# Optimization experiments

Hardware: AMD Instinct MI355X
Metric: run time of the kernel (lower is better)

Reference implementation:

```python
import jax, jax.numpy as jnp
import numpy as np

N, C, E = 2048, 512, 8192
EPS = 1e-5
MASK_FILL = -10000.0


def layer_norm(h, g, b):
    m = jnp.mean(h, axis=-1, keepdims=True)
    v = jnp.mean(jnp.square(h - m), axis=-1, keepdims=True)
    return (h - m) * jax.lax.rsqrt(v + EPS) * g + b


def setup_inputs() -> dict:
    key = jax.random.key(0)
    ks = jax.random.split(key, 20)
    s = 1.0 / np.sqrt(C)
    inp = {
        "x": jax.random.normal(ks[0], (N, C), jnp.float32),
        "edge_index": jax.random.randint(ks[1], (2, E), 0, N, jnp.int64),
        "edge_attr": jax.random.normal(ks[2], (E, C), jnp.float32),
        "edge_masks": jax.random.randint(ks[3], (E, E), 0, 2, jnp.int32).astype(bool),
        # GraphConv.nn: Linear(C, C)
        "W_nn": jax.random.normal(ks[4], (C, C), jnp.float32) * s,
        "b_nn": jax.random.normal(ks[5], (C,), jnp.float32) * s,
        # att_nn: Linear(3C, C) -> Tanh -> Linear(C, 1, bias=False) -> LeakyReLU(0.2)
        "W_att1": jax.random.normal(ks[6], (C, 3 * C), jnp.float32) * (1.0 / np.sqrt(3 * C)),
        "b_att1": jax.random.normal(ks[7], (C,), jnp.float32) * s,
        "w_att2": jax.random.normal(ks[8], (C,), jnp.float32) * s,
        # root weight [C, C] and bias [C]
        "root": jax.random.normal(ks[9], (C, C), jnp.float32) * s,
        "bias": jax.random.normal(ks[10], (C,), jnp.float32) * s,
        # graph_block: LayerNorms + Linear(C, C)
        "gamma1": jnp.ones((C,), jnp.float32),
        "beta1": jnp.zeros((C,), jnp.float32),
        "gamma2": jnp.ones((C,), jnp.float32),
        "beta2": jnp.zeros((C,), jnp.float32),
        "W_lin": jax.random.normal(ks[11], (C, C), jnp.float32) * s,
        "b_lin": jax.random.normal(ks[12], (C,), jnp.float32) * s,
    }
    return inp


def reference(x, edge_index, edge_attr, edge_masks, W_nn, b_nn, W_att1, b_att1,
              w_att2, root, bias, gamma1, beta1, gamma2, beta2, W_lin, b_lin):
    src = edge_index[0]  # x_j (source)
    dst = edge_index[1]  # x_i (target), also aggregation index

    # shared linear on gathered endpoints and edge attrs  [E, C]
    h_i = x[dst] @ W_nn.T + b_nn
    h_j = x[src] @ W_nn.T + b_nn
    h_e = edge_attr @ W_nn.T + b_nn

    # attention MLP (dropout in eval mode = identity)
    cat = jnp.concatenate([h_i, h_j, h_e], axis=1)          # [E, 3C]
    hid = jnp.tanh(cat @ W_att1.T + b_att1)                  # [E, C]
    s = hid @ w_att2                                         # [E]
    s = jax.nn.leaky_relu(s, 0.2)

    # row-wise masked softmax of the broadcast score vector; keep only diagonal
    logits = jnp.where(edge_masks, s[None, :], MASK_FILL)    # [E, E]
    lse = jax.scipy.special.logsumexp(logits, axis=1)        # [E]
    diag_logit = jnp.where(jnp.diagonal(edge_masks), s, MASK_FILL)
    att_diag = jnp.exp(diag_logit - lse)                     # [E]

    msg = h_j * att_diag[:, None]                            # [E, C]
    aggr = jax.ops.segment_sum(msg, dst, num_segments=N)     # [N, C]

    out = aggr + x @ root + bias                             # update()

    # graph_block wrapper
    x1 = layer_norm(out, gamma1, beta1)
    x2 = layer_norm(x1 + (x1 @ W_lin.T + b_lin), gamma2, beta2)
    return x2
```

## Files before the change

### kernel.cpp

```cpp
#include <hip/hip_runtime.h>
#include <stdint.h>
#include <stddef.h>

#define NN 2048
#define CD 512
#define EE 8192

typedef unsigned short u16;
typedef __attribute__((ext_vector_type(8))) short short8;
typedef __attribute__((ext_vector_type(4))) float floatx4;

__device__ inline u16 f2bf(float f) {
    uint32_t u = __float_as_uint(f);
    u += 0x7FFFu + ((u >> 16) & 1u);
    return (u16)(u >> 16);
}
__device__ inline float bf2f(u16 h) { return __uint_as_float(((uint32_t)h) << 16); }

__global__ __launch_bounds__(256) void prep_kernel(
    const float* __restrict__ x, const float* __restrict__ ea,
    const float* __restrict__ Wnn, const float* __restrict__ Wlin,
    const float* __restrict__ root, const float* __restrict__ Watt1,
    u16* __restrict__ xb, u16* __restrict__ eb, u16* __restrict__ Bcat,
    u16* __restrict__ WnnTb, u16* __restrict__ Wlinb, u16* __restrict__ Wpackb)
{
    size_t i4 = ((size_t)blockIdx.x * 256 + threadIdx.x) * 4;
    auto cvt4 = [](const float* src, u16* dst, size_t idx) {
        float4 v = *(const float4*)(src + idx);
        ushort4 o; o.x = f2bf(v.x); o.y = f2bf(v.y); o.z = f2bf(v.z); o.w = f2bf(v.w);
        *(ushort4*)(dst + idx) = o;
    };
    if (i4 < 1048576) { cvt4(x, xb, i4); return; }
    i4 -= 1048576;
    if (i4 < 4194304) { cvt4(ea, eb, i4); return; }
    i4 -= 4194304;
    if (i4 < 262144) { cvt4(Wnn, Bcat, i4); return; }
    i4 -= 262144;
    if (i4 < 262144) {
        int c = (int)(i4 >> 9), k = (int)(i4 & 511);
        ushort4 o;
        o.x = f2bf(root[(size_t)(k + 0) * 512 + c]);
        o.y = f2bf(root[(size_t)(k + 1) * 512 + c]);
        o.z = f2bf(root[(size_t)(k + 2) * 512 + c]);
        o.w = f2bf(root[(size_t)(k + 3) * 512 + c]);
        *(ushort4*)(Bcat + 262144 + i4) = o; return;
    }
    i4 -= 262144;
    if (i4 < 262144) {
        int k = (int)(i4 >> 9), t = (int)(i4 & 511);
        ushort4 o;
        o.x = f2bf(Wnn[(size_t)(t + 0) * 512 + k]);
        o.y = f2bf(Wnn[(size_t)(t + 1) * 512 + k]);
        o.z = f2bf(Wnn[(size_t)(t + 2) * 512 + k]);
        o.w = f2bf(Wnn[(size_t)(t + 3) * 512 + k]);
        *(ushort4*)(WnnTb + i4) = o; return;
    }
    i4 -= 262144;
    if (i4 < 262144) { cvt4(Wlin, Wlinb, i4); return; }
    i4 -= 262144;
    {
        int cp = (int)(i4 >> 9), t = (int)(i4 & 511);
        const float* sp = Watt1 + (size_t)(cp & 511) * 1536 + (cp >> 9) * 512 + t;
        float4 v = *(const float4*)sp;
        ushort4 o; o.x = f2bf(v.x); o.y = f2bf(v.y); o.z = f2bf(v.z); o.w = f2bf(v.w);
        *(ushort4*)(Wpackb + i4) = o;
    }
}

__global__ __launch_bounds__(256) void bbvec_kernel(
    const float* __restrict__ Watt1, const float* __restrict__ bnn,
    const float* __restrict__ batt1, float* __restrict__ bb)
{
    const int c = blockIdx.x, tid = threadIdx.x;
    const float* row = Watt1 + (size_t)c * 1536;
    float partial = 0.0f;
#pragma unroll
    for (int t = tid; t < 1536; t += 256) partial += row[t] * bnn[t & 511];
    for (int o = 32; o; o >>= 1) partial += __shfl_down(partial, o);
    __shared__ float red[4];
    if ((tid & 63) == 0) red[tid >> 6] = partial;
    __syncthreads();
    if (tid == 0) bb[c] = batt1[c] + red[0] + red[1] + red[2] + red[3];
}

template<int BM, int BN>
__device__ inline void gemm_core(const u16* __restrict__ A, const u16* __restrict__ B,
                                 int bm, int bn, int tid, u16* As, u16* Bs,
                                 floatx4 (&acc)[BM / 32][BN / 32])
{
    constexpr int K = 512, BK = 32, WM = BM / 2, WN = BN / 2, FM = WM / 16, FN = WN / 16;
    const int wave = tid >> 6, lane = tid & 63;
    const int wm = wave >> 1, wn = wave & 1;
    const int lrow = lane & 15, lk = lane >> 4;
    constexpr int ALOADS = (BM * BK) / (256 * 8);
    constexpr int BLOADS = (BN * BK) / (256 * 8);
    for (int k0 = 0; k0 < K; k0 += BK) {
        __syncthreads();
#pragma unroll
        for (int c = 0; c < ALOADS; ++c) {
            int e = c * 2048 + tid * 8;
            int row = e >> 5, col = e & 31;
            __builtin_amdgcn_global_load_lds(
                (const __attribute__((address_space(1))) void*)(A + (size_t)(bm * BM + row) * K + k0 + col),
                (__attribute__((address_space(3))) void*)(&As[e]), 16, 0, 0);
        }
#pragma unroll
        for (int c = 0; c < BLOADS; ++c) {
            int e = c * 2048 + tid * 8;
            int row = e >> 5, col = e & 31;
            __builtin_amdgcn_global_load_lds(
                (const __attribute__((address_space(1))) void*)(B + (size_t)(bn * BN + row) * K + k0 + col),
                (__attribute__((address_space(3))) void*)(&Bs[e]), 16, 0, 0);
        }
        __syncthreads();
        short8 af[FM], bfr[FN];
#pragma unroll
        for (int i = 0; i < FM; ++i)
            af[i] = *(const short8*)(&As[(wm * WM + i * 16 + lrow) * BK + lk * 8]);
#pragma unroll
        for (int j = 0; j < FN; ++j)
            bfr[j] = *(const short8*)(&Bs[(wn * WN + j * 16 + lrow) * BK + lk * 8]);
#pragma unroll
        for (int i = 0; i < FM; ++i)
#pragma unroll
            for (int j = 0; j < FN; ++j)
                acc[i][j] = __builtin_amdgcn_mfma_f32_16x16x32_bf16(af[i], bfr[j], acc[i][j], 0, 0, 0);
    }
}

template<int BM, int BN, bool OUT_BF16, bool BIAS>
__global__ __launch_bounds__(256) void gemm_bt(
    const u16* __restrict__ A, const u16* __restrict__ B,
    void* __restrict__ Cout, const float* __restrict__ bias, int Nc)
{
    __shared__ __align__(16) u16 As[BM * 32];
    __shared__ __align__(16) u16 Bs[BN * 32];
    constexpr int WM = BM / 2, WN = BN / 2, FM = WM / 16, FN = WN / 16;
    floatx4 acc[FM][FN] = {};
    const int tid = threadIdx.x, bm = blockIdx.x, bn = blockIdx.y;
    gemm_core<BM, BN>(A, B, bm, bn, tid, As, Bs, acc);
    const int wave = tid >> 6, lane = tid & 63, wm = wave >> 1, wn = wave & 1;
    const int lrow = lane & 15, lk = lane >> 4;
#pragma unroll
    for (int i = 0; i < FM; ++i)
#pragma unroll
        for (int j = 0; j < FN; ++j) {
            const int col = bn * BN + wn * WN + j * 16 + lrow;
            const float bv = BIAS ? bias[col] : 0.0f;
#pragma unroll
            for (int r = 0; r < 4; ++r) {
                const int row = bm * BM + wm * WM + i * 16 + lk * 4 + r;
                const float v = acc[i][j][r] + bv;
                if (OUT_BF16) ((u16*)Cout)[(size_t)row * Nc + col] = f2bf(v);
                else          ((float*)Cout)[(size_t)row * Nc + col] = v;
            }
        }
}

__global__ __launch_bounds__(256) void node_gemm(
    const u16* __restrict__ A, const u16* __restrict__ B,
    const float* __restrict__ bnn, const float* __restrict__ bias,
    u16* __restrict__ Hb, float* __restrict__ OUT1, float* __restrict__ G12)
{
    __shared__ __align__(16) u16 As[128 * 32];
    __shared__ __align__(16) u16 Bs[128 * 32];
    floatx4 acc[4][4] = {};
    const int tid = threadIdx.x, bm = blockIdx.x, bn = blockIdx.y;
    gemm_core<128, 128>(A, B, bm, bn, tid, As, Bs, acc);
    const int wave = tid >> 6, lane = tid & 63, wm = wave >> 1, wn = wave & 1;
    const int lrow = lane & 15, lk = lane >> 4;
#pragma unroll
    for (int i = 0; i < 4; ++i)
#pragma unroll
        for (int j = 0; j < 4; ++j) {
            const int colg = bn * 128 + wn * 64 + j * 16 + lrow;
#pragma unroll
            for (int r = 0; r < 4; ++r) {
                const int row = bm * 128 + wm * 64 + i * 16 + lk * 4 + r;
                const float v = acc[i][j][r];
                if (bn < 4) {
                    Hb[(size_t)row * 512 + colg] = f2bf(v + bnn[colg]);
                } else if (bn < 8) {
                    const int c = colg - 512;
                    OUT1[(size_t)row * 512 + c] = v + bias[c];
                } else {
                    G12[(size_t)row * 1024 + (colg - 1024)] = v;
                }
            }
        }
}

__global__ __launch_bounds__(256) void edge_gemm_score(
    const u16* __restrict__ A, const u16* __restrict__ B,
    const float* __restrict__ G12, const int* __restrict__ ei,
    const float* __restrict__ bb, const float* __restrict__ w2,
    float* __restrict__ sraw)
{
    __shared__ __align__(16) u16 As[128 * 32];
    __shared__ __align__(16) u16 Bs[128 * 32];
    floatx4 acc[4][4] = {};
    const int tid = threadIdx.x, bm = blockIdx.x, bn = blockIdx.y;
    gemm_core<128, 128>(A, B, bm, bn, tid, As, Bs, acc);
    const int wave = tid >> 6, lane = tid & 63, wm = wave >> 1, wn = wave & 1;
    const int lrow = lane & 15, lk = lane >> 4;
#pragma unroll
    for (int i = 0; i < 4; ++i) {
#pragma unroll
        for (int r = 0; r < 4; ++r) {
            const int e = bm * 128 + wm * 64 + i * 16 + lk * 4 + r;
            const int sn = ei[e], dn = ei[EE + e];
            float sp = 0.0f;
#pragma unroll
            for (int j = 0; j < 4; ++j) {
                const int col = bn * 128 + wn * 64 + j * 16 + lrow;
                const float v = acc[i][j][r]
                              + G12[(size_t)dn * 1024 + col]
                              + G12[(size_t)sn * 1024 + 512 + col]
                              + bb[col];
                sp += tanhf(v) * w2[col];
            }
#pragma unroll
            for (int m = 1; m < 16; m <<= 1) sp += __shfl_xor(sp, m);
            if (lrow == 0) atomicAdd(sraw + e, sp);
        }
    }
}

__global__ __launch_bounds__(1024) void softmax_prep(
    const float* __restrict__ sraw, float* __restrict__ p)
{
    const int tid = threadIdx.x;
    float sv[8];
    float m = -3.0e38f;
#pragma unroll
    for (int k = 0; k < 8; ++k) {
        float v = sraw[k * 1024 + tid];
        v = (v >= 0.0f) ? v : 0.2f * v;
        sv[k] = v; m = fmaxf(m, v);
    }
    for (int o = 32; o; o >>= 1) m = fmaxf(m, __shfl_down(m, o));
    __shared__ float red[16];
    if ((tid & 63) == 0) red[tid >> 6] = m;
    __syncthreads();
    float M = red[0];
#pragma unroll
    for (int k = 1; k < 16; ++k) M = fmaxf(M, red[k]);
#pragma unroll
    for (int k = 0; k < 8; ++k) p[k * 1024 + tid] = __expf(sv[k] - M);
}

__global__ __launch_bounds__(256) void lse_att(
    const unsigned char* __restrict__ mask, const float* __restrict__ p,
    float* __restrict__ att)
{
    const int i0 = blockIdx.x * 4, tid = threadIdx.x;
    float sums[4] = {0.0f, 0.0f, 0.0f, 0.0f};
#pragma unroll
    for (int c = 0; c < 2; ++c) {
        const int base = c * 4096 + tid * 16;
        float pv[16];
#pragma unroll
        for (int q = 0; q < 4; ++q)
            *(float4*)(pv + q * 4) = *(const float4*)(p + base + q * 4);
#pragma unroll
        for (int rr = 0; rr < 4; ++rr) {
            uint4 mw = *(const uint4*)(mask + (size_t)(i0 + rr) * EE + base);
            uint32_t w[4] = { mw.x, mw.y, mw.z, mw.w };
            float s = 0.0f;
#pragma unroll
            for (int q = 0; q < 4; ++q) {
                s += pv[q * 4 + 0] * (float)((w[q]      ) & 1u);
                s += pv[q * 4 + 1] * (float)((w[q] >>  8) & 1u);
                s += pv[q * 4 + 2] * (float)((w[q] >> 16) & 1u);
                s += pv[q * 4 + 3] * (float)((w[q] >> 24) & 1u);
            }
            sums[rr] += s;
        }
    }
#pragma unroll
    for (int rr = 0; rr < 4; ++rr)
        for (int o = 32; o; o >>= 1) sums[rr] += __shfl_down(sums[rr], o);
    __shared__ float red[4][4];
    if ((tid & 63) == 0) {
#pragma unroll
        for (int rr = 0; rr < 4; ++rr) red[rr][tid >> 6] = sums[rr];
    }
    __syncthreads();
    if (tid < 4) {
        const int i = i0 + tid;
        const float total = red[tid][0] + red[tid][1] + red[tid][2] + red[tid][3];
        const unsigned char diag = mask[(size_t)i * EE + i];
        float a;
        if (total > 0.0f) a = diag ? (p[i] / total) : 0.0f;
        else              a = 1.0f / (float)EE;
        att[i] = a;
    }
}

__global__ __launch_bounds__(256) void aggr_kernel(
    const u16* __restrict__ Hb, const int* __restrict__ ei,
    const float* __restrict__ att, float* __restrict__ OUT1)
{
    const int e = blockIdx.x;
    const float a = att[e];
    if (a == 0.0f) return;
    const int sn = ei[e], dn = ei[EE + e];
    const u16* h = Hb + (size_t)sn * 512;
    float* o = OUT1 + (size_t)dn * 512;
    const int c = threadIdx.x * 2;
    const uint32_t hv = *(const uint32_t*)(h + c);
    atomicAdd(o + c,     a * bf2f((u16)(hv & 0xffffu)));
    atomicAdd(o + c + 1, a * bf2f((u16)(hv >> 16)));
}

template<bool RESID, bool WRITE_BF16>
__global__ __launch_bounds__(256) void ln_kernel(
    const float* __restrict__ in, const float* __restrict__ resid,
    const float* __restrict__ gamma, const float* __restrict__ beta,
    float* __restrict__ outF, u16* __restrict__ outB)
{
    const int n = blockIdx.x, tid = threadIdx.x;
    const size_t rowoff = (size_t)n * 512;
    float2 v = *(const float2*)(in + rowoff + tid * 2);
    float a0 = v.x, a1 = v.y;
    if (RESID) {
        float2 r = *(const float2*)(resid + rowoff + tid * 2);
        a0 += r.x; a1 += r.y;
    }
    float sum = a0 + a1, sq = a0 * a0 + a1 * a1;
    for (int o = 32; o; o >>= 1) { sum += __shfl_down(sum, o); sq += __shfl_down(sq, o); }
    __shared__ float rs_[4], rq_[4];
    if ((tid & 63) == 0) { rs_[tid >> 6] = sum; rq_[tid >> 6] = sq; }
    __syncthreads();
    sum = rs_[0] + rs_[1] + rs_[2] + rs_[3];
    sq  = rq_[0] + rq_[1] + rq_[2] + rq_[3];
    const float mean = sum * (1.0f / 512.0f);
    const float var  = sq * (1.0f / 512.0f) - mean * mean;
    const float rstd = rsqrtf(var + 1e-5f);
    const int c0 = tid * 2;
    const float y0 = (a0 - mean) * rstd * gamma[c0]     + beta[c0];
    const float y1 = (a1 - mean) * rstd * gamma[c0 + 1] + beta[c0 + 1];
    *(float2*)(outF + rowoff + c0) = make_float2(y0, y1);
    if (WRITE_BF16) { outB[rowoff + c0] = f2bf(y0); outB[rowoff + c0 + 1] = f2bf(y1); }
}

extern "C" void kernel_launch(void* const* d_in, const int* in_sizes, int n_in,
                              void* d_out, int out_size, void* d_ws, size_t ws_size,
                              hipStream_t stream)
{
    const float* x     = (const float*)d_in[0];
    const int*   ei    = (const int*)d_in[1];
    const float* ea    = (const float*)d_in[2];
    const unsigned char* mask = (const unsigned char*)d_in[3];
    const float* Wnn   = (const float*)d_in[4];
    const float* bnn   = (const float*)d_in[5];
    const float* Watt1 = (const float*)d_in[6];
    const float* batt1 = (const float*)d_in[7];
    const float* watt2 = (const float*)d_in[8];
    const float* root  = (const float*)d_in[9];
    const float* bias  = (const float*)d_in[10];
    const float* gam1  = (const float*)d_in[11];
    const float* bet1  = (const float*)d_in[12];
    const float* gam2  = (const float*)d_in[13];
    const float* bet2  = (const float*)d_in[14];
    const float* Wlin  = (const float*)d_in[15];
    const float* blin  = (const float*)d_in[16];
    float* out = (float*)d_out;

    char* w = (char*)d_ws;
    auto take = [&](size_t bytes) -> char* {
        char* pp = w; w += (bytes + 255) & ~(size_t)255; return pp;
    };
    u16*   xb     = (u16*)take((size_t)NN * CD * 2);
    u16*   eb     = (u16*)take((size_t)EE * CD * 2);
    u16*   Wpackb = (u16*)take((size_t)1536 * CD * 2);
    u16*   WnnTb  = (u16*)take((size_t)CD * CD * 2);
    u16*   Wlinb  = (u16*)take((size_t)CD * CD * 2);
    u16*   Bcat   = (u16*)take((size_t)2560 * CD * 2);
    u16*   Hb     = (u16*)take((size_t)NN * CD * 2);
    float* G12    = (float*)take((size_t)NN * 1024 * 4);
    float* OUT1   = (float*)take((size_t)NN * CD * 4);
    float* sraw   = (float*)take((size_t)EE * 4);
    float* pbuf   = (float*)take((size_t)EE * 4);
    float* attb   = (float*)take((size_t)EE * 4);
    float* bb     = (float*)take((size_t)CD * 4);
    float* x1     = (float*)take((size_t)NN * CD * 4);
    u16*   x1b    = (u16*)take((size_t)NN * CD * 2);
    float* Tbuf   = (float*)take((size_t)NN * CD * 4);

    hipMemsetAsync(sraw, 0, (size_t)EE * 4, stream);
    prep_kernel<<<6912, 256, 0, stream>>>(x, ea, Wnn, Wlin, root, Watt1,
                                          xb, eb, Bcat, WnnTb, Wlinb, Wpackb);
    bbvec_kernel<<<512, 256, 0, stream>>>(Watt1, bnn, batt1, bb);
    gemm_bt<64, 128, true, false><<<dim3(24, 4), 256, 0, stream>>>(
        Wpackb, WnnTb, Bcat + (size_t)1024 * 512, nullptr, 512);
    node_gemm<<<dim3(16, 16), 256, 0, stream>>>(xb, Bcat, bnn, bias, Hb, OUT1, G12);
    edge_gemm_score<<<dim3(64, 4), 256, 0, stream>>>(
        eb, Bcat + (size_t)2048 * 512, G12, ei, bb, watt2, sraw);
    softmax_prep<<<1, 1024, 0, stream>>>(sraw, pbuf);
    lse_att<<<2048, 256, 0, stream>>>(mask, pbuf, attb);
    aggr_kernel<<<EE, 256, 0, stream>>>(Hb, ei, attb, OUT1);
    ln_kernel<false, true><<<NN, 256, 0, stream>>>(OUT1, nullptr, gam1, bet1, x1, x1b);
    gemm_bt<64, 128, false, true><<<dim3(32, 4), 256, 0, stream>>>(x1b, Wlinb, Tbuf, blin, 512);
    ln_kernel<true, false><<<NN, 256, 0, stream>>>(Tbuf, x1, gam2, bet2, out, nullptr);
}
```

Before: 457.9 us.

## Fuse softmax, attention and aggregation; full-width edge GEMM; fuse linear with LN2

Folds the bias-vector kernel into the prep kernel and restructures the edge GEMM so each block computes all 512 output columns for 32 edges. That removes the atomic score accumulation and the memset. The separate softmax-max pass is dropped: exp is applied directly to the scores inside a combined LSE/attention/aggregation kernel, which then scatters the messages. The final linear layer is fused with the residual add and the second LayerNorm in one kernel. The aim is fewer launches and fewer intermediate buffers. The cost is lower block counts for the wide-tile GEMMs and no max subtraction, which could overflow exp for large scores.

```diff
diff --git a/kernel.cpp b/kernel.cpp
--- a/kernel.cpp
+++ b/kernel.cpp
@@ -21,9 +21,24 @@
     const float* __restrict__ x, const float* __restrict__ ea,
     const float* __restrict__ Wnn, const float* __restrict__ Wlin,
     const float* __restrict__ root, const float* __restrict__ Watt1,
+    const float* __restrict__ bnn, const float* __restrict__ batt1,
     u16* __restrict__ xb, u16* __restrict__ eb, u16* __restrict__ Bcat,
-    u16* __restrict__ WnnTb, u16* __restrict__ Wlinb, u16* __restrict__ Wpackb)
-{
+    u16* __restrict__ WnnTb, u16* __restrict__ Wlinb, u16* __restrict__ Wpackb,
+    float* __restrict__ bb)
+{
+    if (blockIdx.x >= 6912) {
+        const int c = blockIdx.x - 6912, tid = threadIdx.x;
+        const float* row = Watt1 + (size_t)c * 1536;
+        float partial = 0.0f;
+#pragma unroll
+        for (int t = tid; t < 1536; t += 256) partial += row[t] * bnn[t & 511];
+        for (int o = 32; o; o >>= 1) partial += __shfl_down(partial, o);
+        __shared__ float red[4];
+        if ((tid & 63) == 0) red[tid >> 6] = partial;
+        __syncthreads();
+        if (tid == 0) bb[c] = batt1[c] + red[0] + red[1] + red[2] + red[3];
+        return;
+    }
     size_t i4 = ((size_t)blockIdx.x * 256 + threadIdx.x) * 4;
     auto cvt4 = [](const float* src, u16* dst, size_t idx) {
         float4 v = *(const float4*)(src + idx);
@@ -67,50 +82,56 @@
     }
 }
 
-__global__ __launch_bounds__(256) void bbvec_kernel(
-    const float* __restrict__ Watt1, const float* __restrict__ bnn,
-    const float* __restrict__ batt1, float* __restrict__ bb)
-{
-    const int c = blockIdx.x, tid = threadIdx.x;
-    const float* row = Watt1 + (size_t)c * 1536;
-    float partial = 0.0f;
-#pragma unroll
-    for (int t = tid; t < 1536; t += 256) partial += row[t] * bnn[t & 511];
-    for (int o = 32; o; o >>= 1) partial += __shfl_down(partial, o);
-    __shared__ float red[4];
-    if ((tid & 63) == 0) red[tid >> 6] = partial;
-    __syncthreads();
-    if (tid == 0) bb[c] = batt1[c] + red[0] + red[1] + red[2] + red[3];
-}
-
-template<int BM, int BN>
+template<int BM, int BN, int WR, int WC>
 __device__ inline void gemm_core(const u16* __restrict__ A, const u16* __restrict__ B,
                                  int bm, int bn, int tid, u16* As, u16* Bs,
-                                 floatx4 (&acc)[BM / 32][BN / 32])
-{
-    constexpr int K = 512, BK = 32, WM = BM / 2, WN = BN / 2, FM = WM / 16, FN = WN / 16;
+                                 floatx4 (&acc)[(BM / WR) / 16][(BN / WC) / 16])
+{
+    constexpr int K = 512, BK = 32;
+    constexpr int WM = BM / WR, WN = BN / WC;
+    constexpr int FM = WM / 16, FN = WN / 16;
+    constexpr int ATH = BM * BK / 8;
+    constexpr int BTH = BN * BK / 8;
     const int wave = tid >> 6, lane = tid & 63;
-    const int wm = wave >> 1, wn = wave & 1;
+    const int wm = wave / WC, wn = wave % WC;
     const int lrow = lane & 15, lk = lane >> 4;
-    constexpr int ALOADS = (BM * BK) / (256 * 8);
-    constexpr int BLOADS = (BN * BK) / (256 * 8);
     for (int k0 = 0; k0 < K; k0 += BK) {
         __syncthreads();
-#pragma unroll
-        for (int c = 0; c < ALOADS; ++c) {
-            int e = c * 2048 + tid * 8;
-            int row = e >> 5, col = e & 31;
-            __builtin_amdgcn_global_load_lds(
-                (const __attribute__((address_space(1))) void*)(A + (size_t)(bm * BM + row) * K + k0 + col),
-                (__attribute__((address_space(3))) void*)(&As[e]), 16, 0, 0);
-        }
-#pragma unroll
-        for (int c = 0; c < BLOADS; ++c) {
-            int e = c * 2048 + tid * 8;
-            int row = e >> 5, col = e & 31;
-            __builtin_amdgcn_global_load_lds(
-                (const __attribute__((address_space(1))) void*)(B + (size_t)(bn * BN + row) * K + k0 + col),
-                (__attribute__((address_space(3))) void*)(&Bs[e]), 16, 0, 0);
+        if constexpr (ATH >= 256) {
+#pragma unroll
+            for (int c = 0; c < ATH / 256; ++c) {
+                int e = c * 2048 + tid * 8;
+                int row = e >> 5, col = e & 31;
+                __builtin_amdgcn_global_load_lds(
+                    (const __attribute__((address_space(1))) void*)(A + (size_t)(bm * BM + row) * K + k0 + col),
+                    (__attribute__((address_space(3))) void*)(&As[e]), 16, 0, 0);
+            }
+        } else {
+            if (tid < ATH) {
+                int e = tid * 8;
+                int row = e >> 5, col = e & 31;
+                __builtin_amdgcn_global_load_lds(
+                    (const __attribute__((address_space(1))) void*)(A + (size_t)(bm * BM + row) * K + k0 + col),
+                    (__attribute__((address_space(3))) void*)(&As[e]), 16, 0, 0);
+            }
+        }
+        if constexpr (BTH >= 256) {
+#pragma unroll
+            for (int c = 0; c < BTH / 256; ++c) {
+                int e = c * 2048 + tid * 8;
+                int row = e >> 5, col = e & 31;
+                __builtin_amdgcn_global_load_lds(
+                    (const __attribute__((address_space(1))) void*)(B + (size_t)(bn * BN + row) * K + k0 + col),
+                    (__attribute__((address_space(3))) void*)(&Bs[e]), 16, 0, 0);
+            }
+        } else {
+            if (tid < BTH) {
+                int e = tid * 8;
+                int row = e >> 5, col = e & 31;
+                __builtin_amdgcn_global_load_lds(
+                    (const __attribute__((address_space(1))) void*)(B + (size_t)(bn * BN + row) * K + k0 + col),
+                    (__attribute__((address_space(3))) void*)(&Bs[e]), 16, 0, 0);
+            }
         }
         __syncthreads();
         short8 af[FM], bfr[FN];
@@ -135,21 +156,21 @@
 {
     __shared__ __align__(16) u16 As[BM * 32];
     __shared__ __align__(16) u16 Bs[BN * 32];
-    constexpr int WM = BM / 2, WN = BN / 2, FM = WM / 16, FN = WN / 16;
+    constexpr int FM = (BM / 2) / 16, FN = (BN / 2) / 16;
     floatx4 acc[FM][FN] = {};
     const int tid = threadIdx.x, bm = blockIdx.x, bn = blockIdx.y;
-    gemm_core<BM, BN>(A, B, bm, bn, tid, As, Bs, acc);
+    gemm_core<BM, BN, 2, 2>(A, B, bm, bn, tid, As, Bs, acc);
     const int wave = tid >> 6, lane = tid & 63, wm = wave >> 1, wn = wave & 1;
     const int lrow = lane & 15, lk = lane >> 4;
 #pragma unroll
     for (int i = 0; i < FM; ++i)
 #pragma unroll
         for (int j = 0; j < FN; ++j) {
-            const int col = bn * BN + wn * WN + j * 16 + lrow;
+            const int col = bn * BN + wn * (BN / 2) + j * 16 + lrow;
             const float bv = BIAS ? bias[col] : 0.0f;
 #pragma unroll
             for (int r = 0; r < 4; ++r) {
-                const int row = bm * BM + wm * WM + i * 16 + lk * 4 + r;
+                const int row = bm * BM + wm * (BM / 2) + i * 16 + lk * 4 + r;
                 const float v = acc[i][j][r] + bv;
                 if (OUT_BF16) ((u16*)Cout)[(size_t)row * Nc + col] = f2bf(v);
                 else          ((float*)Cout)[(size_t)row * Nc + col] = v;
@@ -166,7 +187,7 @@
     __shared__ __align__(16) u16 Bs[128 * 32];
     floatx4 acc[4][4] = {};
     const int tid = threadIdx.x, bm = blockIdx.x, bn = blockIdx.y;
-    gemm_core<128, 128>(A, B, bm, bn, tid, As, Bs, acc);
+    gemm_core<128, 128, 2, 2>(A, B, bm, bn, tid, As, Bs, acc);
     const int wave = tid >> 6, lane = tid & 63, wm = wave >> 1, wn = wave & 1;
     const int lrow = lane & 15, lk = lane >> 4;
 #pragma unroll
@@ -194,64 +215,47 @@
     const u16* __restrict__ A, const u16* __restrict__ B,
     const float* __restrict__ G12, const int* __restrict__ ei,
     const float* __restrict__ bb, const float* __restrict__ w2,
-    float* __restrict__ sraw)
-{
-    __shared__ __align__(16) u16 As[128 * 32];
-    __shared__ __align__(16) u16 Bs[128 * 32];
-    floatx4 acc[4][4] = {};
-    const int tid = threadIdx.x, bm = blockIdx.x, bn = blockIdx.y;
-    gemm_core<128, 128>(A, B, bm, bn, tid, As, Bs, acc);
-    const int wave = tid >> 6, lane = tid & 63, wm = wave >> 1, wn = wave & 1;
+    float* __restrict__ sOut)
+{
+    __shared__ __align__(16) u16 As[32 * 32];
+    __shared__ __align__(16) u16 Bs[512 * 32];
+    __shared__ float sred[32][4];
+    floatx4 acc[2][8] = {};
+    const int tid = threadIdx.x, bm = blockIdx.x;
+    gemm_core<32, 512, 1, 4>(A, B, bm, 0, tid, As, Bs, acc);
+    const int wave = tid >> 6, lane = tid & 63;
     const int lrow = lane & 15, lk = lane >> 4;
 #pragma unroll
-    for (int i = 0; i < 4; ++i) {
+    for (int i = 0; i < 2; ++i) {
 #pragma unroll
         for (int r = 0; r < 4; ++r) {
-            const int e = bm * 128 + wm * 64 + i * 16 + lk * 4 + r;
+            const int e = bm * 32 + i * 16 + lk * 4 + r;
             const int sn = ei[e], dn = ei[EE + e];
+            const float* gd = G12 + (size_t)dn * 1024;
+            const float* gs = G12 + (size_t)sn * 1024 + 512;
             float sp = 0.0f;
 #pragma unroll
-            for (int j = 0; j < 4; ++j) {
-                const int col = bn * 128 + wn * 64 + j * 16 + lrow;
-                const float v = acc[i][j][r]
-                              + G12[(size_t)dn * 1024 + col]
-                              + G12[(size_t)sn * 1024 + 512 + col]
-                              + bb[col];
+            for (int j = 0; j < 8; ++j) {
+                const int col = wave * 128 + j * 16 + lrow;
+                const float v = acc[i][j][r] + gd[col] + gs[col] + bb[col];
                 sp += tanhf(v) * w2[col];
             }
 #pragma unroll
             for (int m = 1; m < 16; m <<= 1) sp += __shfl_xor(sp, m);
-            if (lrow == 0) atomicAdd(sraw + e, sp);
-        }
-    }
-}
-
-__global__ __launch_bounds__(1024) void softmax_prep(
-    const float* __restrict__ sraw, float* __restrict__ p)
-{
-    const int tid = threadIdx.x;
-    float sv[8];
-    float m = -3.0e38f;
-#pragma unroll
-    for (int k = 0; k < 8; ++k) {
-        float v = sraw[k * 1024 + tid];
-        v = (v >= 0.0f) ? v : 0.2f * v;
-        sv[k] = v; m = fmaxf(m, v);
-    }
-    for (int o = 32; o; o >>= 1) m = fmaxf(m, __shfl_down(m, o));
-    __shared__ float red[16];
-    if ((tid & 63) == 0) red[tid >> 6] = m;
-    __syncthreads();
-    float M = red[0];
-#pragma unroll
-    for (int k = 1; k < 16; ++k) M = fmaxf(M, red[k]);
-#pragma unroll
-    for (int k = 0; k < 8; ++k) p[k * 1024 + tid] = __expf(sv[k] - M);
-}
-
-__global__ __launch_bounds__(256) void lse_att(
-    const unsigned char* __restrict__ mask, const float* __restrict__ p,
-    float* __restrict__ att)
+            if (lrow == 0) sred[i * 16 + lk * 4 + r][wave] = sp;
+        }
+    }
+    __syncthreads();
+    if (tid < 32) {
+        float s = sred[tid][0] + sred[tid][1] + sred[tid][2] + sred[tid][3];
+        sOut[bm * 32 + tid] = (s >= 0.0f) ? s : 0.2f * s;
+    }
+}
+
+__global__ __launch_bounds__(256) void lse_att_aggr(
+    const unsigned char* __restrict__ mask, const float* __restrict__ s,
+    const int* __restrict__ ei, const u16* __restrict__ Hb,
+    float* __restrict__ OUT1)
 {
     const int i0 = blockIdx.x * 4, tid = threadIdx.x;
     float sums[4] = {0.0f, 0.0f, 0.0f, 0.0f};
@@ -260,27 +264,31 @@
         const int base = c * 4096 + tid * 16;
         float pv[16];
 #pragma unroll
-        for (int q = 0; q < 4; ++q)
-            *(float4*)(pv + q * 4) = *(const float4*)(p + base + q * 4);
+        for (int q = 0; q < 4; ++q) {
+            float4 sv = *(const float4*)(s + base + q * 4);
+            pv[q * 4 + 0] = __expf(sv.x); pv[q * 4 + 1] = __expf(sv.y);
+            pv[q * 4 + 2] = __expf(sv.z); pv[q * 4 + 3] = __expf(sv.w);
+        }
 #pragma unroll
         for (int rr = 0; rr < 4; ++rr) {
             uint4 mw = *(const uint4*)(mask + (size_t)(i0 + rr) * EE + base);
             uint32_t w[4] = { mw.x, mw.y, mw.z, mw.w };
-            float s = 0.0f;
+            float acc = 0.0f;
 #pragma unroll
             for (int q = 0; q < 4; ++q) {
-                s += pv[q * 4 + 0] * (float)((w[q]      ) & 1u);
-                s += pv[q * 4 + 1] * (float)((w[q] >>  8) & 1u);
-                s += pv[q * 4 + 2] * (float)((w[q] >> 16) & 1u);
-                s += pv[q * 4 + 3] * (float)((w[q] >> 24) & 1u);
-            }
-            sums[rr] += s;
+                acc += pv[q * 4 + 0] * (float)((w[q]      ) & 1u);
+                acc += pv[q * 4 + 1] * (float)((w[q] >>  8) & 1u);
+                acc += pv[q * 4 + 2] * (float)((w[q] >> 16) & 1u);
+                acc += pv[q * 4 + 3] * (float)((w[q] >> 24) & 1u);
+            }
+            sums[rr] += acc;
         }
     }
 #pragma unroll
     for (int rr = 0; rr < 4; ++rr)
         for (int o = 32; o; o >>= 1) sums[rr] += __shfl_down(sums[rr], o);
     __shared__ float red[4][4];
+    __shared__ float attv[4];
     if ((tid & 63) == 0) {
 #pragma unroll
         for (int rr = 0; rr < 4; ++rr) red[rr][tid >> 6] = sums[rr];
@@ -291,26 +299,24 @@
         const float total = red[tid][0] + red[tid][1] + red[tid][2] + red[tid][3];
         const unsigned char diag = mask[(size_t)i * EE + i];
         float a;
-        if (total > 0.0f) a = diag ? (p[i] / total) : 0.0f;
+        if (total > 0.0f) a = diag ? (__expf(s[i]) / total) : 0.0f;
         else              a = 1.0f / (float)EE;
-        att[i] = a;
-    }
-}
-
-__global__ __launch_bounds__(256) void aggr_kernel(
-    const u16* __restrict__ Hb, const int* __restrict__ ei,
-    const float* __restrict__ att, float* __restrict__ OUT1)
-{
-    const int e = blockIdx.x;
-    const float a = att[e];
-    if (a == 0.0f) return;
-    const int sn = ei[e], dn = ei[EE + e];
-    const u16* h = Hb + (size_t)sn * 512;
-    float* o = OUT1 + (size_t)dn * 512;
-    const int c = threadIdx.x * 2;
-    const uint32_t hv = *(const uint32_t*)(h + c);
-    atomicAdd(o + c,     a * bf2f((u16)(hv & 0xffffu)));
-    atomicAdd(o + c + 1, a * bf2f((u16)(hv >> 16)));
+        attv[tid] = a;
+    }
+    __syncthreads();
+#pragma unroll
+    for (int rr = 0; rr < 4; ++rr) {
+        const float a = attv[rr];
+        if (a == 0.0f) continue;
+        const int e = i0 + rr;
+        const int sn = ei[e], dn = ei[EE + e];
+        const u16* h = Hb + (size_t)sn * 512;
+        float* o = OUT1 + (size_t)dn * 512;
+        const int c2 = tid * 2;
+        const uint32_t hv = *(const uint32_t*)(h + c2);
+        atomicAdd(o + c2,     a * bf2f((u16)(hv & 0xffffu)));
+        atomicAdd(o + c2 + 1, a * bf2f((u16)(hv >> 16)));
+    }
 }
 
 template<bool RESID, bool WRITE_BF16>
@@ -342,6 +348,65 @@
     const float y1 = (a1 - mean) * rstd * gamma[c0 + 1] + beta[c0 + 1];
     *(float2*)(outF + rowoff + c0) = make_float2(y0, y1);
     if (WRITE_BF16) { outB[rowoff + c0] = f2bf(y0); outB[rowoff + c0 + 1] = f2bf(y1); }
+}
+
+__global__ __launch_bounds__(256) void lin_ln2(
+    const u16* __restrict__ x1b, const u16* __restrict__ Wlinb,
+    const float* __restrict__ x1, const float* __restrict__ blin,
+    const float* __restrict__ gam2, const float* __restrict__ bet2,
+    float* __restrict__ out)
+{
+    __shared__ __align__(16) u16 As[16 * 32];
+    __shared__ __align__(16) u16 Bs[512 * 32];
+    __shared__ float rsum[4][16], rsq[4][16], rmean[16], rrstd[16];
+    floatx4 acc[1][8] = {};
+    const int tid = threadIdx.x, bm = blockIdx.x;
+    gemm_core<16, 512, 1, 4>(x1b, Wlinb, bm, 0, tid, As, Bs, acc);
+    const int wave = tid >> 6, lane = tid & 63;
+    const int lrow = lane & 15, lk = lane >> 4;
+    float psum[4] = {0, 0, 0, 0}, psq[4] = {0, 0, 0, 0};
+#pragma unroll
+    for (int j = 0; j < 8; ++j) {
+        const int col = wave * 128 + j * 16 + lrow;
+        const float bl = blin[col];
+#pragma unroll
+        for (int r = 0; r < 4; ++r) {
+            const int grow = bm * 16 + lk * 4 + r;
+            const float v = acc[0][j][r] + bl + x1[(size_t)grow * 512 + col];
+            acc[0][j][r] = v;
+            psum[r] += v; psq[r] += v * v;
+        }
+    }
+#pragma unroll
+    for (int r = 0; r < 4; ++r) {
+#pragma unroll
+        for (int m = 1; m < 16; m <<= 1) {
+            psum[r] += __shfl_xor(psum[r], m);
+            psq[r]  += __shfl_xor(psq[r], m);
+        }
+        if (lrow == 0) { rsum[wave][lk * 4 + r] = psum[r]; rsq[wave][lk * 4 + r] = psq[r]; }
+    }
+    __syncthreads();
+    if (tid < 16) {
+        const float sm = rsum[0][tid] + rsum[1][tid] + rsum[2][tid] + rsum[3][tid];
+        const float sq = rsq[0][tid] + rsq[1][tid] + rsq[2][tid] + rsq[3][tid];
+        const float mean = sm * (1.0f / 512.0f);
+        const float var  = sq * (1.0f / 512.0f) - mean * mean;
+        rmean[tid] = mean;
+        rrstd[tid] = rsqrtf(var + 1e-5f);
+    }
+    __syncthreads();
+#pragma unroll
+    for (int j = 0; j < 8; ++j) {
+        const int col = wave * 128 + j * 16 + lrow;
+        const float g = gam2[col], b = bet2[col];
+#pragma unroll
+        for (int r = 0; r < 4; ++r) {
+            const int row16 = lk * 4 + r;
+            out[(size_t)(bm * 16 + row16) * 512 + col] =
+                (acc[0][j][r] - rmean[row16]) * rrstd[row16] * g + b;
+        }
+    }
 }
 
 extern "C" void kernel_launch(void* const* d_in, const int* in_sizes, int n_in,
@@ -380,27 +445,19 @@
     u16*   Hb     = (u16*)take((size_t)NN * CD * 2);
     float* G12    = (float*)take((size_t)NN * 1024 * 4);
     float* OUT1   = (float*)take((size_t)NN * CD * 4);
-    float* sraw   = (float*)take((size_t)EE * 4);
-    float* pbuf   = (float*)take((size_t)EE * 4);
-    float* attb   = (float*)take((size_t)EE * 4);
+    float* sbuf   = (float*)take((size_t)EE * 4);
     float* bb     = (float*)take((size_t)CD * 4);
     float* x1     = (float*)take((size_t)NN * CD * 4);
     u16*   x1b    = (u16*)take((size_t)NN * CD * 2);
-    float* Tbuf   = (float*)take((size_t)NN * CD * 4);
-
-    hipMemsetAsync(sraw, 0, (size_t)EE * 4, stream);
-    prep_kernel<<<6912, 256, 0, stream>>>(x, ea, Wnn, Wlin, root, Watt1,
-                                          xb, eb, Bcat, WnnTb, Wlinb, Wpackb);
-    bbvec_kernel<<<512, 256, 0, stream>>>(Watt1, bnn, batt1, bb);
+
+    prep_kernel<<<7424, 256, 0, stream>>>(x, ea, Wnn, Wlin, root, Watt1, bnn, batt1,
+                                          xb, eb, Bcat, WnnTb, Wlinb, Wpackb, bb);
     gemm_bt<64, 128, true, false><<<dim3(24, 4), 256, 0, stream>>>(
         Wpackb, WnnTb, Bcat + (size_t)1024 * 512, nullptr, 512);
     node_gemm<<<dim3(16, 16), 256, 0, stream>>>(xb, Bcat, bnn, bias, Hb, OUT1, G12);
-    edge_gemm_score<<<dim3(64, 4), 256, 0, stream>>>(
-        eb, Bcat + (size_t)2048 * 512, G12, ei, bb, watt2, sraw);
-    softmax_prep<<<1, 1024, 0, stream>>>(sraw, pbuf);
-    lse_att<<<2048, 256, 0, stream>>>(mask, pbuf, attb);
-    aggr_kernel<<<EE, 256, 0, stream>>>(Hb, ei, attb, OUT1);
+    edge_gemm_score<<<256, 256, 0, stream>>>(
+        eb, Bcat + (size_t)2048 * 512, G12, ei, bb, watt2, sbuf);
+    lse_att_aggr<<<2048, 256, 0, stream>>>(mask, sbuf, ei, Hb, OUT1);
     ln_kernel<false, true><<<NN, 256, 0, stream>>>(OUT1, nullptr, gam1, bet1, x1, x1b);
-    gemm_bt<64, 128, false, true><<<dim3(32, 4), 256, 0, stream>>>(x1b, Wlinb, Tbuf, blin, 512);
-    ln_kernel<true, false><<<NN, 256, 0, stream>>>(Tbuf, x1, gam2, bet2, out, nullptr);
-}
+    lin_ln2<<<128, 256, 0, stream>>>(x1b, Wlinb, x1, blin, gam2, bet2, out);
+}
```

Measured after the change: 451.2 us. No clear change (-1.5%).
